# Optimization experiments

Measured on AMD Instinct MI355X. Metric: run time of the kernel, lower is better.

Reference implementation:

```python
import jax, jax.numpy as jnp
import numpy as np

B, S, H, D, BS = 4, 1024, 32, 128, 16  # batch, seq, heads, head_dim, block_size
E = H * D  # 4096 hidden
NB = S // BS  # blocks per sequence


def _rope(x, cos, sin):
    # x: [T, H, D]; cos/sin: [T, D//2]  (GPT-NeoX half-split rotary)
    d2 = x.shape[-1] // 2
    x1, x2 = x[..., :d2], x[..., d2:]
    c, s = cos[:, None, :], sin[:, None, :]
    return jnp.concatenate([x1 * c - x2 * s, x2 * c + x1 * s], axis=-1)


def setup_inputs() -> dict:
    key = jax.random.key(0)
    ks = jax.random.split(key, 6)
    hidden_states = jax.random.normal(ks[0], (B * S, E), jnp.float32)
    qkv_weight = jax.random.normal(ks[1], (3, E, E), jnp.float32) * 0.02
    o_weight = jax.random.normal(ks[2], (E, E), jnp.float32) * 0.02
    # rotary tables per token position (sequences are contiguous, equal length)
    inv_freq = 1.0 / (10000.0 ** (jnp.arange(0, D, 2, dtype=jnp.float32) / D))
    pos = jnp.tile(jnp.arange(S, dtype=jnp.float32), B)  # [T]
    ang = pos[:, None] * inv_freq[None, :]  # [T, D//2]
    cos, sin = jnp.cos(ang), jnp.sin(ang)
    k_cache = jnp.zeros((B * NB, H, BS, D), jnp.float32)
    v_cache = jnp.zeros((B * NB, H, BS, D), jnp.float32)
    block_tables = jnp.arange(B * NB, dtype=jnp.int32).reshape(B, NB)
    cu_seqlens = (jnp.arange(B + 1, dtype=jnp.int32) * S)
    sequence_lengths = jnp.full((B,), S, dtype=jnp.int32)
    return {"hidden_states": hidden_states, "qkv_weight": qkv_weight, "o_weight": o_weight,
            "cos": cos, "sin": sin, "k_cache": k_cache, "v_cache": v_cache,
            "block_tables": block_tables, "cu_seqlens": cu_seqlens,
            "sequence_lengths": sequence_lengths}


def reference(hidden_states, qkv_weight, o_weight, cos, sin, k_cache, v_cache,
              block_tables, cu_seqlens, sequence_lengths):
    T = hidden_states.shape[0]
    # fused QKV projection: bmm of [3,T,E] x [3,E,E]
    qkv = jnp.einsum('te,kef->ktf', hidden_states, qkv_weight).reshape(3, T, H, D)
    q, k, v = qkv[0], qkv[1], qkv[2]
    # rotary embedding on q, k
    q = _rope(q, cos, sin)
    k = _rope(k, cos, sin)
    # paged KV-cache memcpy: write k/v into [num_blocks, H, BS, D] via block_tables
    k_blk = k.reshape(B, NB, BS, H, D).transpose(0, 1, 3, 2, 4).reshape(B * NB, H, BS, D)
    v_blk = v.reshape(B, NB, BS, H, D).transpose(0, 1, 3, 2, 4).reshape(B * NB, H, BS, D)
    bt = block_tables.reshape(-1)
    k_cache = k_cache.at[bt].set(k_blk)
    v_cache = v_cache.at[bt].set(v_blk)
    # varlen causal attention (equal-length sequences -> batched causal attention)
    qb = q.reshape(B, S, H, D)
    kb = k.reshape(B, S, H, D)
    vb = v.reshape(B, S, H, D)
    sm_scale = 1.0 / jnp.sqrt(jnp.float32(D))
    scores = jnp.einsum('bqhd,bkhd->bhqk', qb, kb) * sm_scale
    causal = jnp.tril(jnp.ones((S, S), bool))
    scores = jnp.where(causal[None, None], scores, jnp.finfo(scores.dtype).min)
    probs = jax.nn.softmax(scores, axis=-1)
    attn = jnp.einsum('bhqk,bkhd->bqhd', probs, vb).reshape(T, E)
    out = attn @ o_weight  # o_proj (bias-free linear)
    return out, k_cache, v_cache
```

## Files before the change

kernel.cpp:

```cpp
#include <hip/hip_runtime.h>

#define B_  4
#define S_  1024
#define H_  32
#define D_  128
#define E_  4096
#define T_  4096
#define NB_ 64
#define BS_ 16
#define NT_ 128

typedef __attribute__((ext_vector_type(8))) __bf16 bf16x8;
typedef __attribute__((ext_vector_type(4))) __bf16 bf16x4;
typedef __attribute__((ext_vector_type(4))) float f32x4;

__device__ __forceinline__ void gload_lds16(const __bf16* g, __bf16* l) {
  __builtin_amdgcn_global_load_lds((const __attribute__((address_space(1))) void*)g,
                                   (__attribute__((address_space(3))) void*)l, 16, 0, 0);
}

__global__ __launch_bounds__(256) void k_convert_hs(const float* __restrict__ x,
                                                    __bf16* __restrict__ y, int n4) {
  int i = blockIdx.x * 256 + threadIdx.x;
  if (i < n4) {
    float4 v = ((const float4*)x)[i];
    bf16x4 o;
    o[0] = (__bf16)v.x; o[1] = (__bf16)v.y; o[2] = (__bf16)v.z; o[3] = (__bf16)v.w;
    ((bf16x4*)y)[i] = o;
  }
}

__global__ __launch_bounds__(256) void k_transpose_w(const float* __restrict__ W,
                                                     __bf16* __restrict__ WT) {
  __shared__ float tile[32][33];
  const float* Wm = W + (size_t)blockIdx.z * E_ * E_;
  __bf16* WTm = WT + (size_t)blockIdx.z * E_ * E_;
  int e0 = blockIdx.x * 32, f0 = blockIdx.y * 32;
  int tx = threadIdx.x & 31, ty = threadIdx.x >> 5;
  for (int i = ty; i < 32; i += 8) tile[i][tx] = Wm[(size_t)(e0 + i) * E_ + f0 + tx];
  __syncthreads();
  for (int i = ty; i < 32; i += 8) WTm[(size_t)(f0 + i) * E_ + e0 + tx] = (__bf16)tile[tx][i];
}

__global__ __launch_bounds__(256) void k_transpose_v(const __bf16* __restrict__ v,
                                                     __bf16* __restrict__ vT) {
  __shared__ __bf16 tile[32][33];
  size_t bh = blockIdx.z;
  const __bf16* vp = v + bh * S_ * D_;
  __bf16* vtp = vT + bh * S_ * D_;
  int s0 = blockIdx.x * 32, d0 = blockIdx.y * 32;
  int tx = threadIdx.x & 31, ty = threadIdx.x >> 5;
  for (int i = ty; i < 32; i += 8) tile[i][tx] = vp[(size_t)(s0 + i) * D_ + d0 + tx];
  __syncthreads();
  for (int i = ty; i < 32; i += 8) vtp[(size_t)(d0 + i) * S_ + s0 + tx] = tile[tx][i];
}

__global__ __launch_bounds__(256) void k_rope(__bf16* __restrict__ q, __bf16* __restrict__ k,
                                              const __bf16* __restrict__ v,
                                              const float* __restrict__ cosb,
                                              const float* __restrict__ sinb,
                                              const int* __restrict__ bt,
                                              float* __restrict__ kc, float* __restrict__ vc) {
  int idx = blockIdx.x * 256 + threadIdx.x;
  int j = idx & 63;
  int s = (idx >> 6) & (S_ - 1);
  int h = (idx >> 16) & (H_ - 1);
  int b = idx >> 21;
  size_t base = (((size_t)b * H_ + h) * S_ + s) * D_;
  float c  = cosb[(size_t)(b * S_ + s) * 64 + j];
  float sn = sinb[(size_t)(b * S_ + s) * 64 + j];
  float q1 = (float)q[base + j], q2 = (float)q[base + j + 64];
  float k1 = (float)k[base + j], k2 = (float)k[base + j + 64];
  float q1n = q1 * c - q2 * sn, q2n = q2 * c + q1 * sn;
  float k1n = k1 * c - k2 * sn, k2n = k2 * c + k1 * sn;
  q[base + j] = (__bf16)q1n; q[base + j + 64] = (__bf16)q2n;
  k[base + j] = (__bf16)k1n; k[base + j + 64] = (__bf16)k2n;
  int nb = s >> 4, sb = s & 15;
  int blk = bt[b * NB_ + nb];
  size_t cidx = (((size_t)blk * H_ + h) * BS_ + sb) * D_;
  kc[cidx + j] = k1n; kc[cidx + j + 64] = k2n;
  vc[cidx + j] = (float)v[base + j];
  vc[cidx + j + 64] = (float)v[base + j + 64];
}


#define STAGE256(tt) {                                                             \
    int _b = (tt) & 3;                                                             \
    const __bf16* _ag = Ag + (size_t)(tt) * 32;                                    \
    const __bf16* _bg = Bg + (size_t)(tt) * 32;                                    \
    __bf16* _al = &ring[_b][0][0] + wid * 512 + lane * 8;                          \
    __bf16* _bl = &ring[_b][1][0] + wid * 512 + lane * 8;                          \
    gload_lds16(_ag, _al);                                                         \
    gload_lds16(_ag + (size_t)128 * E_, _al + 4096);                               \
    gload_lds16(_bg, _bl);                                                         \
    gload_lds16(_bg + (size_t)128 * E_, _bl + 4096);                               \
  }

#define COMPUTE256(tt) {                                                           \
    int _b = (tt) & 3;                                                             \
    const __bf16* _ab = &ring[_b][0][0];                                           \
    const __bf16* _bb = &ring[_b][1][0];                                           \
    bf16x8 afr[8], bfr[4];                                                         \
    _Pragma("unroll")                                                              \
    for (int i = 0; i < 8; i++)                                                    \
      afr[i] = *(const bf16x8*)&_ab[(wm * 128 + i * 16 + l15) * 32 + rdoff];       \
    _Pragma("unroll")                                                              \
    for (int j = 0; j < 4; j++)                                                    \
      bfr[j] = *(const bf16x8*)&_bb[(wn * 64 + j * 16 + l15) * 32 + rdoff];        \
    __builtin_amdgcn_s_setprio(1);                                                 \
    _Pragma("unroll")                                                              \
    for (int i = 0; i < 8; i++)                                                    \
      _Pragma("unroll")                                                            \
      for (int j = 0; j < 4; j++)                                                  \
        acc[i][j] = __builtin_amdgcn_mfma_f32_16x16x32_bf16(afr[i], bfr[j], acc[i][j], 0, 0, 0); \
    __builtin_amdgcn_s_setprio(0);                                                 \
  }

#define GEMM256_BODY                                                               \
  __shared__ __align__(16) __bf16 ring[4][2][256 * 32];               \
  int tid = threadIdx.x;                                                           \
  int wid = tid >> 6, lane = tid & 63, l15 = lane & 15, quad = lane >> 4;          \
  int wm = wid >> 2, wn = wid & 3;                                                 \
  int rdoff = (quad ^ ((l15 >> 1) & 3)) * 8;          \
                               \
  int cpx = (int)gridDim.x >> 3;                                                   \
  int wg = ((int)blockIdx.x & 7) * cpx + ((int)blockIdx.x >> 3);                   \
  int m0 = (wg & 15) * 256, n0 = (wg >> 4) * 256;                                  \
  int srow = wid * 16 + (lane >> 2);                                               \
  int scol = (((lane & 3) ^ ((lane >> 3) & 3)) * 8);   \
  const __bf16* Ag = A + (size_t)(m0 + srow) * E_ + scol;                          \
  const __bf16* Bg = BT + (size_t)(n0 + srow) * E_ + scol;                         \
  f32x4 acc[8][4] = {};                                                            \
  STAGE256(0) STAGE256(1) STAGE256(2)                                              \
  for (int t = 0; t < NT_; ++t) {                                                  \
    if (t < NT_ - 2)       { asm volatile("s_waitcnt vmcnt(8)" ::: "memory"); }    \
    else if (t == NT_ - 2) { asm volatile("s_waitcnt vmcnt(4)" ::: "memory"); }    \
    else                   { asm volatile("s_waitcnt vmcnt(0)" ::: "memory"); }    \
    __builtin_amdgcn_s_barrier();                                                  \
    if (t + 3 < NT_) STAGE256(t + 3)                                               \
    COMPUTE256(t)                                                                  \
  }

__global__ __launch_bounds__(512, 1) void k_gemm_qkv(const __bf16* __restrict__ A,
                                                     const __bf16* __restrict__ BT,
                                                     __bf16* __restrict__ qkvb) {
  GEMM256_BODY
  for (int i = 0; i < 8; i++) {
    int tbase = m0 + wm * 128 + i * 16 + quad * 4;
    for (int j = 0; j < 4; j++) {
      int n = n0 + wn * 64 + j * 16 + l15;
      int kk = n >> 12, nl = n & 4095;
      int h = nl >> 7, d = nl & 127;
      for (int r = 0; r < 4; r++) {
        int t = tbase + r;
        int bb = t >> 10, s = t & 1023;
        size_t idx = ((((size_t)kk * B_ + bb) * H_ + h) * S_ + s) * D_ + d;
        qkvb[idx] = (__bf16)acc[i][j][r];
      }
    }
  }
}

__global__ __launch_bounds__(512, 1) void k_gemm_out(const __bf16* __restrict__ A,
                                                     const __bf16* __restrict__ BT,
                                                     float* __restrict__ out) {
  GEMM256_BODY
  for (int i = 0; i < 8; i++) {
    int tbase = m0 + wm * 128 + i * 16 + quad * 4;
    for (int j = 0; j < 4; j++) {
      int n = n0 + wn * 64 + j * 16 + l15;
      for (int r = 0; r < 4; r++)
        out[(size_t)(tbase + r) * E_ + n] = acc[i][j][r];
    }
  }
}

__global__ __launch_bounds__(256) void k_attn(const __bf16* __restrict__ q,
                                              const __bf16* __restrict__ k,
                                              const __bf16* __restrict__ vT,
                                              __bf16* __restrict__ attn) {
  __shared__ __align__(16) __bf16 Qs[64][136];
  __shared__ __align__(16) __bf16 Ks[64][136];
  __shared__ __align__(16) __bf16 Vs[128][72];
  __shared__ __align__(16) __bf16 Ps[4][16][72];

  int q0 = blockIdx.x * 64;
  int h = blockIdx.y, b = blockIdx.z;
  int tid = threadIdx.x, wid = tid >> 6, lane = tid & 63, l15 = lane & 15, quad = lane >> 4;

  size_t bh = (size_t)b * H_ + h;
  const __bf16* Qp = q + bh * S_ * D_;
  const __bf16* Kp = k + bh * S_ * D_;
  const __bf16* Vp = vT + bh * (size_t)D_ * S_;

  for (int c = tid; c < 1024; c += 256) {
    int r = c >> 4, dp = (c & 15) * 8;
    *(int4*)&Qs[r][dp] = *(const int4*)&Qp[(size_t)(q0 + r) * D_ + dp];
  }
  __syncthreads();
  bf16x8 aq[4];
  for (int ks = 0; ks < 4; ks++) aq[ks] = *(const bf16x8*)&Qs[wid * 16 + l15][ks * 32 + quad * 8];

  float m_run[4], l_run[4];
  f32x4 o_acc[8] = {};
  for (int r = 0; r < 4; r++) { m_run[r] = -1e30f; l_run[r] = 0.f; }
  const float sm_scale = 0.08838834764831845f;

  int kend = q0 + 64;
  for (int sk0 = 0; sk0 < kend; sk0 += 64) {
    __syncthreads();
    for (int c = tid; c < 1024; c += 256) {
      int r = c >> 4, dp = (c & 15) * 8;
      *(int4*)&Ks[r][dp] = *(const int4*)&Kp[(size_t)(sk0 + r) * D_ + dp];
    }
    for (int c = tid; c < 1024; c += 256) {
      int d = c >> 3, sp = (c & 7) * 8;
      *(int4*)&Vs[d][sp] = *(const int4*)&Vp[(size_t)d * S_ + sk0 + sp];
    }
    __syncthreads();

    f32x4 st[4] = {};
    for (int nt = 0; nt < 4; nt++)
      for (int ks = 0; ks < 4; ks++) {
        bf16x8 bk = *(const bf16x8*)&Ks[nt * 16 + l15][ks * 32 + quad * 8];
        st[nt] = __builtin_amdgcn_mfma_f32_16x16x32_bf16(aq[ks], bk, st[nt], 0, 0, 0);
      }

    int qg = q0 + wid * 16 + quad * 4;
    float mnew[4], alpha[4];
    for (int r = 0; r < 4; r++) {
      float rmax = -1e30f;
      for (int nt = 0; nt < 4; nt++) {
        int kg = sk0 + nt * 16 + l15;
        float vsc = st[nt][r] * sm_scale;
        if (kg > qg + r) vsc = -1e30f;
        st[nt][r] = vsc;
        rmax = fmaxf(rmax, vsc);
      }
      for (int off = 1; off < 16; off <<= 1) rmax = fmaxf(rmax, __shfl_xor(rmax, off));
      mnew[r] = fmaxf(m_run[r], rmax);
      alpha[r] = __expf(m_run[r] - mnew[r]);
      float s_ = 0.f;
      for (int nt = 0; nt < 4; nt++) {
        float p = __expf(st[nt][r] - mnew[r]);
        st[nt][r] = p;
        s_ += p;
      }
      for (int off = 1; off < 16; off <<= 1) s_ += __shfl_xor(s_, off);
      l_run[r] = l_run[r] * alpha[r] + s_;
      m_run[r] = mnew[r];
    }

    for (int nt = 0; nt < 4; nt++)
      for (int r = 0; r < 4; r++)
        Ps[wid][quad * 4 + r][nt * 16 + l15] = (__bf16)st[nt][r];

    for (int dt = 0; dt < 8; dt++)
      for (int r = 0; r < 4; r++)
        o_acc[dt][r] *= alpha[r];

    __syncthreads();

    for (int ks2 = 0; ks2 < 2; ks2++) {
      bf16x8 ap = *(const bf16x8*)&Ps[wid][l15][ks2 * 32 + quad * 8];
      for (int dt = 0; dt < 8; dt++) {
        bf16x8 bv = *(const bf16x8*)&Vs[dt * 16 + l15][ks2 * 32 + quad * 8];
        o_acc[dt] = __builtin_amdgcn_mfma_f32_16x16x32_bf16(ap, bv, o_acc[dt], 0, 0, 0);
      }
    }
  }

  size_t trow = (size_t)b * S_ + q0 + wid * 16 + quad * 4;
  for (int dt = 0; dt < 8; dt++) {
    int e = h * D_ + dt * 16 + l15;
    for (int r = 0; r < 4; r++) {
      float val = o_acc[dt][r] / l_run[r];
      attn[(trow + r) * E_ + e] = (__bf16)val;
    }
  }
}

extern "C" void kernel_launch(void* const* d_in, const int* in_sizes, int n_in,
                              void* d_out, int out_size, void* d_ws, size_t ws_size,
                              hipStream_t stream) {
  const float* hs    = (const float*)d_in[0];
  const float* qkv_w = (const float*)d_in[1];
  const float* o_w   = (const float*)d_in[2];
  const float* cosb  = (const float*)d_in[3];
  const float* sinb  = (const float*)d_in[4];
  const int*   bt    = (const int*)d_in[7];

  float* out = (float*)d_out;
  float* kc  = out + (size_t)T_ * E_;
  float* vc  = kc + (size_t)B_ * NB_ * H_ * BS_ * D_;

  char* ws = (char*)d_ws;
  __bf16* hsb  = (__bf16*)ws;
  __bf16* wT   = (__bf16*)(ws + 33554432);
  __bf16* oT   = wT + (size_t)3 * E_ * E_;
  __bf16* qb   = (__bf16*)(ws + 167772160);
  __bf16* kb   = qb + (size_t)B_ * H_ * S_ * D_;
  __bf16* vb   = kb + (size_t)B_ * H_ * S_ * D_;
  __bf16* vTt  = (__bf16*)(ws + 268435456);
  __bf16* attn = hsb;

  k_convert_hs<<<dim3(T_ * E_ / 4 / 256), dim3(256), 0, stream>>>(hs, hsb, T_ * E_ / 4);
  k_transpose_w<<<dim3(128, 128, 3), dim3(256), 0, stream>>>(qkv_w, wT);
  k_transpose_w<<<dim3(128, 128, 1), dim3(256), 0, stream>>>(o_w, oT);
  k_gemm_qkv<<<dim3(768), dim3(512), 0, stream>>>(hsb, wT, qb);
  k_rope<<<dim3(32768), dim3(256), 0, stream>>>(qb, kb, vb, cosb, sinb, bt, kc, vc);
  k_transpose_v<<<dim3(32, 4, 128), dim3(256), 0, stream>>>(vb, vTt);
  k_attn<<<dim3(16, 32, 4), dim3(256), 0, stream>>>(qb, kb, vTt, attn);
  k_gemm_out<<<dim3(256), dim3(512), 0, stream>>>(attn, oT, out);
}
```

Baseline: 1.329 ms.

## Interleave A-fragment LDS reads with MFMAs and vectorize weight transpose

The GEMM inner step now loads A fragments from LDS two rows at a time, prefetching the next pair while the current pair feeds MFMAs, with a sched_barrier to hold that order. This is meant to hide LDS read latency behind matrix math and lower register pressure from holding all eight A fragments. The weight transpose kernel now uses float4 loads and 4-wide bf16 stores instead of scalar accesses. The sched_barrier may stop the compiler from finding a better schedule, and the transposed LDS reads may hit bank conflicts.

```diff
diff --git a/kernel.cpp b/kernel.cpp
--- a/kernel.cpp
+++ b/kernel.cpp
@@ -36,10 +36,17 @@
   const float* Wm = W + (size_t)blockIdx.z * E_ * E_;
   __bf16* WTm = WT + (size_t)blockIdx.z * E_ * E_;
   int e0 = blockIdx.x * 32, f0 = blockIdx.y * 32;
-  int tx = threadIdx.x & 31, ty = threadIdx.x >> 5;
-  for (int i = ty; i < 32; i += 8) tile[i][tx] = Wm[(size_t)(e0 + i) * E_ + f0 + tx];
+  int r = threadIdx.x >> 3, c = threadIdx.x & 7;
+  float4 v = *(const float4*)&Wm[(size_t)(e0 + r) * E_ + f0 + c * 4];
+  tile[r][c * 4 + 0] = v.x; tile[r][c * 4 + 1] = v.y;
+  tile[r][c * 4 + 2] = v.z; tile[r][c * 4 + 3] = v.w;
   __syncthreads();
-  for (int i = ty; i < 32; i += 8) WTm[(size_t)(f0 + i) * E_ + e0 + tx] = (__bf16)tile[tx][i];
+  bf16x4 o;
+  o[0] = (__bf16)tile[c * 4 + 0][r];
+  o[1] = (__bf16)tile[c * 4 + 1][r];
+  o[2] = (__bf16)tile[c * 4 + 2][r];
+  o[3] = (__bf16)tile[c * 4 + 3][r];
+  *(bf16x4*)&WTm[(size_t)(f0 + r) * E_ + e0 + c * 4] = o;
 }
 
 __global__ __launch_bounds__(256) void k_transpose_v(const __bf16* __restrict__ v,
@@ -98,21 +105,30 @@
 
 #define COMPUTE256(tt) {                                                           \
     int _b = (tt) & 3;                                                             \
-    const __bf16* _ab = &ring[_b][0][0];                                           \
-    const __bf16* _bb = &ring[_b][1][0];                                           \
-    bf16x8 afr[8], bfr[4];                                                         \
+    const __bf16* _ab = &ring[_b][0][0] + (wm * 128 + l15) * 32 + rdoff;           \
+    const __bf16* _bb = &ring[_b][1][0] + (wn * 64 + l15) * 32 + rdoff;            \
+    bf16x8 bfr[4];                                                                 \
     _Pragma("unroll")                                                              \
-    for (int i = 0; i < 8; i++)                                                    \
-      afr[i] = *(const bf16x8*)&_ab[(wm * 128 + i * 16 + l15) * 32 + rdoff];       \
-    _Pragma("unroll")                                                              \
-    for (int j = 0; j < 4; j++)                                                    \
-      bfr[j] = *(const bf16x8*)&_bb[(wn * 64 + j * 16 + l15) * 32 + rdoff];        \
+    for (int j = 0; j < 4; j++) bfr[j] = *(const bf16x8*)&_bb[j * 512];            \
+    bf16x8 a0 = *(const bf16x8*)&_ab[0];                                           \
+    bf16x8 a1 = *(const bf16x8*)&_ab[512];                                         \
     __builtin_amdgcn_s_setprio(1);                                                 \
     _Pragma("unroll")                                                              \
-    for (int i = 0; i < 8; i++)                                                    \
+    for (int p = 0; p < 4; p++) {                                                  \
+      bf16x8 n0 = {}, n1 = {};                                                     \
+      if (p < 3) {                                                                 \
+        n0 = *(const bf16x8*)&_ab[(2 * p + 2) * 512];                              \
+        n1 = *(const bf16x8*)&_ab[(2 * p + 3) * 512];                              \
+      }                                                                            \
       _Pragma("unroll")                                                            \
       for (int j = 0; j < 4; j++)                                                  \
-        acc[i][j] = __builtin_amdgcn_mfma_f32_16x16x32_bf16(afr[i], bfr[j], acc[i][j], 0, 0, 0); \
+        acc[2 * p][j] = __builtin_amdgcn_mfma_f32_16x16x32_bf16(a0, bfr[j], acc[2 * p][j], 0, 0, 0); \
+      _Pragma("unroll")                                                            \
+      for (int j = 0; j < 4; j++)                                                  \
+        acc[2 * p + 1][j] = __builtin_amdgcn_mfma_f32_16x16x32_bf16(a1, bfr[j], acc[2 * p + 1][j], 0, 0, 0); \
+      __builtin_amdgcn_sched_barrier(0);                                           \
+      if (p < 3) { a0 = n0; a1 = n1; }                                             \
+    }                                                                              \
     __builtin_amdgcn_s_setprio(0);                                                 \
   }
 
```

After: 1.300 ms. 1.02x faster.
